# Kernel optimization log

Hardware: AMD Instinct MI355X
Metric: run time of the kernel (lower is better)

## Reference

```python
import jax, jax.numpy as jnp
import numpy as np

B, N, C_IN = 2048, 62, 512
NUM_LAYERS, H, C_OUT_PER_HEAD = 3, 8, 64


def setup_inputs() -> dict:
    key = jax.random.key(0)
    k1, k2, k3, k4 = jax.random.split(key, 4)
    x = jax.random.normal(k1, (B, N, C_IN), dtype=jnp.float32)
    L = jax.random.uniform(k2, (N, N), dtype=jnp.float32)
    W_alphas = jax.random.normal(k3, (NUM_LAYERS, H, C_IN, N), dtype=jnp.float32) * 0.05
    W = jax.random.normal(k4, (NUM_LAYERS, H, C_IN, C_OUT_PER_HEAD), dtype=jnp.float32) * 0.05
    return {"x": x, "L": L, "W_alphas": W_alphas, "W": W}


def reference(x, L, W_alphas, W):
    # x: [B, N, C]; L: [N, N]; W_alphas: [Lyr, H, C, N]; W: [Lyr, H, C, Co]
    num_layers = W_alphas.shape[0]
    n = x.shape[1]
    I = jnp.eye(n, dtype=x.dtype)
    # Chebyshev-style adjacency powers: [I, L, L@L, ...]
    adjs = [I, L]
    for _ in range(2, num_layers):
        adjs.append(adjs[-1] @ L)
    adjs = adjs[:num_layers]

    result = None
    for l in range(num_layers):
        A = adjs[l]
        A_hat = A + I
        D = A.sum(axis=-1)                      # [N]
        d_neg = jnp.where(D == 0, 0.0, 1.0 / D)  # torch: D^-1 with inf -> 0
        # attention logits per head: D_neg @ (x @ W_alphas[h]) -> [H, B, N, N]
        a = jnp.einsum('bnc,hcm->hbnm', x, W_alphas[l])
        a = d_neg[:, None] * a                   # diag(D_neg) @ M == row scaling
        a = jax.nn.leaky_relu(a, 0.01)
        a = jax.nn.softmax(a, axis=-2)           # softmax over rows (dim=-2)
        ax = jnp.einsum('nm,bmc->bnc', A_hat, x)  # A_hat @ x, shared across heads
        o = jnp.einsum('hbnm,bmc->hbnc', a, ax)
        o = jnp.einsum('hbnc,hco->hbno', o, W[l])
        o = jax.nn.relu(o)
        # concat heads along feature dim (head-major order, matching torch.cat)
        o = jnp.moveaxis(o, 0, 2).reshape(o.shape[1], n, -1)  # [B, N, H*Co]
        result = o if result is None else result + o
    return jax.nn.relu(result)
```

## Files before the change

### kernel.cpp

```cpp
#include <hip/hip_runtime.h>


using f32x4 = __attribute__((ext_vector_type(4))) float;
using s16x8 = __attribute__((ext_vector_type(8))) short;

__device__ __forceinline__ unsigned short f2bf(float f){
  unsigned int u = __builtin_bit_cast(unsigned int, f);
  u += 0x7fffu + ((u >> 16) & 1u);
  return (unsigned short)(u >> 16);
}
__device__ __forceinline__ float bf2f(unsigned short h){
  unsigned int u = ((unsigned int)h) << 16;
  return __builtin_bit_cast(float, u);
}
__device__ __forceinline__ f32x4 zf4(){ f32x4 v; v[0]=0.f; v[1]=0.f; v[2]=0.f; v[3]=0.f; return v; }

__device__ __forceinline__ void async16(const void* g, void* l){
  __builtin_amdgcn_global_load_lds((const __attribute__((address_space(1))) unsigned int*)g,
                                   (__attribute__((address_space(3))) unsigned int*)l,
                                   16, 0, 0);
}

__global__ void k_prep_adj(const float* __restrict__ L,
                           unsigned short* __restrict__ ahat,
                           float* __restrict__ dneg)
{
  __shared__ float Ls[62*62];
  __shared__ float A2s[62*62];
  const int tid = threadIdx.x;
  for (int i = tid; i < 62*62; i += 256) Ls[i] = L[i];
  __syncthreads();
  for (int i = tid; i < 62*62; i += 256){
    const int n = i / 62, m = i % 62;
    float s = 0.f;
    for (int k = 0; k < 62; ++k) s += Ls[n*62 + k] * Ls[k*62 + m];
    A2s[i] = s;
  }
  __syncthreads();
  for (int i = tid; i < 3*64*64; i += 256){
    const int l = i >> 12, r = i & 4095, n = r >> 6, m = r & 63;
    float v = 0.f;
    if (n < 62 && m < 62){
      float base = 0.f;
      if (l == 0) base = (n == m) ? 1.f : 0.f;
      else if (l == 1) base = Ls[n*62 + m];
      else base = A2s[n*62 + m];
      v = base + ((n == m) ? 1.f : 0.f);
    }
    ahat[i] = f2bf(v);
  }
  for (int i = tid; i < 3*64; i += 256){
    const int l = i >> 6, n = i & 63;
    float D = 0.f;
    if (n < 62){
      if (l == 0) D = 1.f;
      else {
        const float* src = (l == 1) ? Ls : A2s;
        for (int m = 0; m < 62; ++m) D += src[n*62 + m];
      }
    }
    dneg[i] = (D == 0.f) ? 0.f : 1.f / D;
  }
}

__global__ void k_prep_w(const float* __restrict__ Wa, const float* __restrict__ W,
                         unsigned short* __restrict__ WaT, unsigned short* __restrict__ WT)
{
  const int idx = blockIdx.x * 256 + threadIdx.x;
  if (idx < 786432){
    const int c = idx & 511, m = (idx >> 9) & 63, lh = idx >> 15;
    const float v = (m < 62) ? Wa[((size_t)lh*512 + c)*62 + m] : 0.f;
    WaT[idx] = f2bf(v);
  } else if (idx < 1572864){
    const int j = idx - 786432;
    const int c = j & 511, o = (j >> 9) & 63, lh = j >> 15;
    WT[j] = f2bf(W[((size_t)lh*512 + c)*64 + o]);
  }
}

#define LP 72

__global__ __launch_bounds__(256, 2)
void k_main(const float* __restrict__ x,
            const unsigned short* __restrict__ WaT,
            const unsigned short* __restrict__ WT,
            const unsigned short* __restrict__ ahat,
            const float* __restrict__ dneg,
            float* __restrict__ out)
{
  __shared__ __align__(16) unsigned short s_u[16384];
  __shared__ __align__(16) float s_dneg[192];
  __shared__ __align__(16) float s_red[256];
  __shared__ __align__(16) float s_red2[256];

  unsigned short* const s_chunk0 = s_u;
  unsigned short* const s_chunk1 = s_u + 8192;
  unsigned short* const s_a      = s_u;
  unsigned short* const s_xwT    = s_u + 4608;
  unsigned short* const s_axwT   = s_u + 9216;

  const int tid  = threadIdx.x;
  const int wv   = tid >> 6;
  const int lane = tid & 63;
  const int q    = lane >> 4;
  const int m15  = lane & 15;
  const int b    = blockIdx.x;
  const int r0   = 16*wv + 4*q;

  if (tid < 192) s_dneg[tid] = dneg[tid];

  s16x8 afr[16];
  {
    const int row = 16*wv + m15;
    if (row < 62){
      const float* xp = x + ((size_t)b*62 + row)*512 + q*8;
      #pragma unroll
      for (int kk = 0; kk < 16; ++kk){
        const f32x4 f0 = *(const f32x4*)(xp + kk*32);
        const f32x4 f1 = *(const f32x4*)(xp + kk*32 + 4);
        s16x8 t;
        t[0]=(short)f2bf(f0[0]); t[1]=(short)f2bf(f0[1]); t[2]=(short)f2bf(f0[2]); t[3]=(short)f2bf(f0[3]);
        t[4]=(short)f2bf(f1[0]); t[5]=(short)f2bf(f1[1]); t[6]=(short)f2bf(f1[2]); t[7]=(short)f2bf(f1[3]);
        afr[kk] = t;
      }
    } else {
      #pragma unroll
      for (int kk = 0; kk < 16; ++kk){
        s16x8 t; t[0]=0;t[1]=0;t[2]=0;t[3]=0;t[4]=0;t[5]=0;t[6]=0;t[7]=0; afr[kk] = t;
      }
    }
  }

  #pragma unroll 1
  for (int h = 0; h < 8; ++h){
    f32x4 out_acc[4];
    #pragma unroll
    for (int ct = 0; ct < 4; ++ct) out_acc[ct] = zf4();

    #pragma unroll 1
    for (int l = 0; l < 3; ++l){
      const int lh = l*8 + h;
      const unsigned short* wa_base = WaT + (size_t)lh*32768;
      const unsigned short* wt_base = WT  + (size_t)lh*32768;

      f32x4 accL[4], accX[4];
      #pragma unroll
      for (int ct = 0; ct < 4; ++ct){ accL[ct] = zf4(); accX[ct] = zf4(); }

      #pragma unroll
      for (int kc = 0; kc < 4; ++kc){
        __syncthreads();
        #pragma unroll
        for (int tt = 0; tt < 4; ++tt){
          const int n  = 16*tt + 4*wv + q;
          const int jl = m15 ^ (n & 15);
          const size_t goff = (size_t)n*512 + (size_t)kc*128 + (size_t)jl*8;
          const int    loff = tt*2048 + wv*512 + lane*8;
          async16(wa_base + goff, s_chunk0 + loff);
          async16(wt_base + goff, s_chunk1 + loff);
        }
        __syncthreads();
        #pragma unroll
        for (int ks = 0; ks < 4; ++ks){
          const s16x8 a = afr[kc*4 + ks];
          #pragma unroll
          for (int ct = 0; ct < 4; ++ct){
            const int off = (16*ct + m15)*128 + (((4*ks + q) ^ m15) * 8);
            const s16x8 bL = *(const s16x8*)(s_chunk0 + off);
            const s16x8 bX = *(const s16x8*)(s_chunk1 + off);
            accL[ct] = __builtin_amdgcn_mfma_f32_16x16x32_bf16(a, bL, accL[ct], 0, 0, 0);
            accX[ct] = __builtin_amdgcn_mfma_f32_16x16x32_bf16(a, bX, accX[ct], 0, 0, 0);
          }
        }
      }
      __syncthreads();

      {
        const f32x4 dn = *(const f32x4*)(&s_dneg[l*64 + r0]);
        #pragma unroll
        for (int ct = 0; ct < 4; ++ct){
          const int col = 16*ct + m15;
          #pragma unroll
          for (int r = 0; r < 4; ++r){
            const int n = r0 + r;
            float v = accL[ct][r] * dn[r];
            v = (v > 0.f) ? v : 0.01f*v;
            if (n >= 62) v = -1e30f;
            s_a[n*LP + col]   = f2bf(v);
            s_xwT[col*LP + n] = f2bf(accX[ct][r]);
          }
        }
      }
      __syncthreads();

      f32x4 accA[4];
      #pragma unroll
      for (int ct = 0; ct < 4; ++ct) accA[ct] = zf4();
      #pragma unroll
      for (int ks = 0; ks < 2; ++ks){
        const s16x8 aA = *(const s16x8*)(ahat + (size_t)(l*64 + 16*wv + m15)*64 + ks*32 + q*8);
        #pragma unroll
        for (int ct = 0; ct < 4; ++ct){
          const s16x8 bA = *(const s16x8*)(&s_xwT[(16*ct + m15)*LP + ks*32 + q*8]);
          accA[ct] = __builtin_amdgcn_mfma_f32_16x16x32_bf16(aA, bA, accA[ct], 0, 0, 0);
        }
      }
      #pragma unroll
      for (int ct = 0; ct < 4; ++ct){
        #pragma unroll
        for (int r = 0; r < 4; ++r)
          s_axwT[(16*ct + m15)*LP + (r0 + r)] = f2bf(accA[ct][r]);
      }

      float vsm[16];
      float mp = -3.0e38f;
      #pragma unroll
      for (int i = 0; i < 16; ++i){
        vsm[i] = bf2f(s_a[(16*wv + i)*LP + lane]);
        mp = fmaxf(mp, vsm[i]);
      }
      s_red[wv*64 + lane] = mp;
      __syncthreads();
      const float mc = fmaxf(fmaxf(s_red[lane], s_red[64 + lane]),
                             fmaxf(s_red[128 + lane], s_red[192 + lane]));
      float ev[16]; float sp = 0.f;
      #pragma unroll
      for (int i = 0; i < 16; ++i){ ev[i] = __expf(vsm[i] - mc); sp += ev[i]; }
      s_red2[wv*64 + lane] = sp;
      __syncthreads();
      const float sc = s_red2[lane] + s_red2[64 + lane] + s_red2[128 + lane] + s_red2[192 + lane];
      const float inv = 1.0f / sc;
      #pragma unroll
      for (int i = 0; i < 16; ++i)
        s_a[(16*wv + i)*LP + lane] = f2bf(ev[i] * inv);
      __syncthreads();

      f32x4 accO[4];
      #pragma unroll
      for (int ct = 0; ct < 4; ++ct) accO[ct] = zf4();
      #pragma unroll
      for (int ks = 0; ks < 2; ++ks){
        const s16x8 aO = *(const s16x8*)(&s_a[(16*wv + m15)*LP + ks*32 + q*8]);
        #pragma unroll
        for (int ct = 0; ct < 4; ++ct){
          const s16x8 bO = *(const s16x8*)(&s_axwT[(16*ct + m15)*LP + ks*32 + q*8]);
          accO[ct] = __builtin_amdgcn_mfma_f32_16x16x32_bf16(aO, bO, accO[ct], 0, 0, 0);
        }
      }
      #pragma unroll
      for (int ct = 0; ct < 4; ++ct){
        #pragma unroll
        for (int r = 0; r < 4; ++r)
          out_acc[ct][r] += fmaxf(accO[ct][r], 0.f);
      }
    }

    #pragma unroll
    for (int ct = 0; ct < 4; ++ct){
      const int col = h*64 + 16*ct + m15;
      #pragma unroll
      for (int r = 0; r < 4; ++r){
        const int n = r0 + r;
        if (n < 62)
          out[((size_t)b*62 + n)*512 + col] = fmaxf(out_acc[ct][r], 0.f);
      }
    }
  }
}

extern "C" void kernel_launch(void* const* d_in, const int* in_sizes, int n_in,
                              void* d_out, int out_size, void* d_ws, size_t ws_size,
                              hipStream_t stream)
{
  const float* x  = (const float*)d_in[0];
  const float* L  = (const float*)d_in[1];
  const float* Wa = (const float*)d_in[2];
  const float* W  = (const float*)d_in[3];
  float* out = (float*)d_out;

  char* ws = (char*)d_ws;
  unsigned short* ws_ahat = (unsigned short*)(ws);
  float*          ws_dneg = (float*)(ws + 24576);
  unsigned short* ws_WaT  = (unsigned short*)(ws + 25600);
  unsigned short* ws_WT   = (unsigned short*)(ws + 25600 + 1572864);

  k_prep_adj<<<1, 256, 0, stream>>>(L, ws_ahat, ws_dneg);
  k_prep_w<<<6144, 256, 0, stream>>>(Wa, W, ws_WaT, ws_WT);
  k_main<<<2048, 256, 0, stream>>>(x, ws_WaT, ws_WT, ws_ahat, ws_dneg, out);
}
```

Measured before the change: 1.070 ms.

## Process two batch elements per block sharing staged weight chunks

Each block now runs 512 threads as two 4-wave groups, each handling a different batch element. The groups cooperatively stage the shared Wa and W chunks into LDS, one group loading each, so every weight chunk fetched from global memory serves two batch elements and the per-block load work halves. Per-group scratch regions for the attention, xW and A·xW tiles are placed in separate LDS slices, and the softmax reductions are indexed per group. In exchange the block is larger, LDS use rises, and block-wide barriers now couple both groups, which may lower occupancy.

```diff
diff --git a/kernel.cpp b/kernel.cpp
--- a/kernel.cpp
+++ b/kernel.cpp
@@ -80,7 +80,7 @@
 
 #define LP 72
 
-__global__ __launch_bounds__(256, 2)
+__global__ __launch_bounds__(512, 2)
 void k_main(const float* __restrict__ x,
             const unsigned short* __restrict__ WaT,
             const unsigned short* __restrict__ WT,
@@ -88,30 +88,33 @@
             const float* __restrict__ dneg,
             float* __restrict__ out)
 {
-  __shared__ __align__(16) unsigned short s_u[16384];
+  __shared__ __align__(16) unsigned short s_u[27648];
   __shared__ __align__(16) float s_dneg[192];
-  __shared__ __align__(16) float s_red[256];
-  __shared__ __align__(16) float s_red2[256];
+  __shared__ __align__(16) float s_red[512];
+  __shared__ __align__(16) float s_red2[512];
 
   unsigned short* const s_chunk0 = s_u;
   unsigned short* const s_chunk1 = s_u + 8192;
-  unsigned short* const s_a      = s_u;
-  unsigned short* const s_xwT    = s_u + 4608;
-  unsigned short* const s_axwT   = s_u + 9216;
 
   const int tid  = threadIdx.x;
-  const int wv   = tid >> 6;
+  const int wv8  = tid >> 6;
+  const int grp  = wv8 >> 2;
+  const int wvg  = wv8 & 3;
   const int lane = tid & 63;
   const int q    = lane >> 4;
   const int m15  = lane & 15;
-  const int b    = blockIdx.x;
-  const int r0   = 16*wv + 4*q;
+  const int b    = 2*blockIdx.x + grp;
+  const int r0   = 16*wvg + 4*q;
+
+  unsigned short* const s_a    = s_u + grp*13824;
+  unsigned short* const s_xwT  = s_u + grp*13824 + 4608;
+  unsigned short* const s_axwT = s_u + grp*13824 + 9216;
 
   if (tid < 192) s_dneg[tid] = dneg[tid];
 
   s16x8 afr[16];
   {
-    const int row = 16*wv + m15;
+    const int row = 16*wvg + m15;
     if (row < 62){
       const float* xp = x + ((size_t)b*62 + row)*512 + q*8;
       #pragma unroll
@@ -140,8 +143,8 @@
     #pragma unroll 1
     for (int l = 0; l < 3; ++l){
       const int lh = l*8 + h;
-      const unsigned short* wa_base = WaT + (size_t)lh*32768;
-      const unsigned short* wt_base = WT  + (size_t)lh*32768;
+      const unsigned short* g_base = (grp ? WT : WaT) + (size_t)lh*32768;
+      unsigned short* const  l_base = grp ? s_chunk1 : s_chunk0;
 
       f32x4 accL[4], accX[4];
       #pragma unroll
@@ -152,12 +155,11 @@
         __syncthreads();
         #pragma unroll
         for (int tt = 0; tt < 4; ++tt){
-          const int n  = 16*tt + 4*wv + q;
+          const int n  = 16*tt + 4*wvg + q;
           const int jl = m15 ^ (n & 15);
           const size_t goff = (size_t)n*512 + (size_t)kc*128 + (size_t)jl*8;
-          const int    loff = tt*2048 + wv*512 + lane*8;
-          async16(wa_base + goff, s_chunk0 + loff);
-          async16(wt_base + goff, s_chunk1 + loff);
+          const int    loff = tt*2048 + wvg*512 + lane*8;
+          async16(g_base + goff, l_base + loff);
         }
         __syncthreads();
         #pragma unroll
@@ -198,7 +200,7 @@
       for (int ct = 0; ct < 4; ++ct) accA[ct] = zf4();
       #pragma unroll
       for (int ks = 0; ks < 2; ++ks){
-        const s16x8 aA = *(const s16x8*)(ahat + (size_t)(l*64 + 16*wv + m15)*64 + ks*32 + q*8);
+        const s16x8 aA = *(const s16x8*)(ahat + (size_t)(l*64 + 16*wvg + m15)*64 + ks*32 + q*8);
         #pragma unroll
         for (int ct = 0; ct < 4; ++ct){
           const s16x8 bA = *(const s16x8*)(&s_xwT[(16*ct + m15)*LP + ks*32 + q*8]);
@@ -216,23 +218,24 @@
       float mp = -3.0e38f;
       #pragma unroll
       for (int i = 0; i < 16; ++i){
-        vsm[i] = bf2f(s_a[(16*wv + i)*LP + lane]);
+        vsm[i] = bf2f(s_a[(16*wvg + i)*LP + lane]);
         mp = fmaxf(mp, vsm[i]);
       }
-      s_red[wv*64 + lane] = mp;
-      __syncthreads();
-      const float mc = fmaxf(fmaxf(s_red[lane], s_red[64 + lane]),
-                             fmaxf(s_red[128 + lane], s_red[192 + lane]));
+      s_red[wv8*64 + lane] = mp;
+      __syncthreads();
+      const int rb = grp*256 + lane;
+      const float mc = fmaxf(fmaxf(s_red[rb], s_red[64 + rb]),
+                             fmaxf(s_red[128 + rb], s_red[192 + rb]));
       float ev[16]; float sp = 0.f;
       #pragma unroll
       for (int i = 0; i < 16; ++i){ ev[i] = __expf(vsm[i] - mc); sp += ev[i]; }
-      s_red2[wv*64 + lane] = sp;
-      __syncthreads();
-      const float sc = s_red2[lane] + s_red2[64 + lane] + s_red2[128 + lane] + s_red2[192 + lane];
+      s_red2[wv8*64 + lane] = sp;
+      __syncthreads();
+      const float sc = s_red2[rb] + s_red2[64 + rb] + s_red2[128 + rb] + s_red2[192 + rb];
       const float inv = 1.0f / sc;
       #pragma unroll
       for (int i = 0; i < 16; ++i)
-        s_a[(16*wv + i)*LP + lane] = f2bf(ev[i] * inv);
+        s_a[(16*wvg + i)*LP + lane] = f2bf(ev[i] * inv);
       __syncthreads();
 
       f32x4 accO[4];
@@ -240,7 +243,7 @@
       for (int ct = 0; ct < 4; ++ct) accO[ct] = zf4();
       #pragma unroll
       for (int ks = 0; ks < 2; ++ks){
-        const s16x8 aO = *(const s16x8*)(&s_a[(16*wv + m15)*LP + ks*32 + q*8]);
+        const s16x8 aO = *(const s16x8*)(&s_a[(16*wvg + m15)*LP + ks*32 + q*8]);
         #pragma unroll
         for (int ct = 0; ct < 4; ++ct){
           const s16x8 bO = *(const s16x8*)(&s_axwT[(16*ct + m15)*LP + ks*32 + q*8]);
@@ -286,5 +289,5 @@
 
   k_prep_adj<<<1, 256, 0, stream>>>(L, ws_ahat, ws_dneg);
   k_prep_w<<<6144, 256, 0, stream>>>(Wa, W, ws_WaT, ws_WT);
-  k_main<<<2048, 256, 0, stream>>>(x, ws_WaT, ws_WT, ws_ahat, ws_dneg, out);
-}
+  k_main<<<1024, 512, 0, stream>>>(x, ws_WaT, ws_WT, ws_ahat, ws_dneg, out);
+}
```

Result: slower. 1.138 ms (+6.3%).

## Fold softmax normalization into A_hat·XW output and drop max subtraction

Applied to the files above, without the earlier changes.

Computes exp of the leaky-relu logits directly without subtracting the column max, and instead of normalizing the attention matrix, it scales the A_hat·(xW) rows by the reciprocal column sums before the final MFMA. This removes one reduction pass, one barrier and a rewrite of the attention tile, and packs four bf16 values per 64-bit shared-memory store. It also launches the adjacency prep kernel with 1024 threads. Skipping the max subtraction risks overflow if logits grow large.

```diff
diff --git a/kernel.cpp b/kernel.cpp
--- a/kernel.cpp
+++ b/kernel.cpp
@@ -15,6 +15,13 @@
 }
 __device__ __forceinline__ f32x4 zf4(){ f32x4 v; v[0]=0.f; v[1]=0.f; v[2]=0.f; v[3]=0.f; return v; }
 
+__device__ __forceinline__ unsigned long long pack4bf(float a, float b, float c, float d){
+  return (unsigned long long)f2bf(a)
+       | ((unsigned long long)f2bf(b) << 16)
+       | ((unsigned long long)f2bf(c) << 32)
+       | ((unsigned long long)f2bf(d) << 48);
+}
+
 __device__ __forceinline__ void async16(const void* g, void* l){
   __builtin_amdgcn_global_load_lds((const __attribute__((address_space(1))) unsigned int*)g,
                                    (__attribute__((address_space(3))) unsigned int*)l,
@@ -28,16 +35,17 @@
   __shared__ float Ls[62*62];
   __shared__ float A2s[62*62];
   const int tid = threadIdx.x;
-  for (int i = tid; i < 62*62; i += 256) Ls[i] = L[i];
+  const int NT  = blockDim.x;
+  for (int i = tid; i < 62*62; i += NT) Ls[i] = L[i];
   __syncthreads();
-  for (int i = tid; i < 62*62; i += 256){
+  for (int i = tid; i < 62*62; i += NT){
     const int n = i / 62, m = i % 62;
     float s = 0.f;
     for (int k = 0; k < 62; ++k) s += Ls[n*62 + k] * Ls[k*62 + m];
     A2s[i] = s;
   }
   __syncthreads();
-  for (int i = tid; i < 3*64*64; i += 256){
+  for (int i = tid; i < 3*64*64; i += NT){
     const int l = i >> 12, r = i & 4095, n = r >> 6, m = r & 63;
     float v = 0.f;
     if (n < 62 && m < 62){
@@ -49,7 +57,7 @@
     }
     ahat[i] = f2bf(v);
   }
-  for (int i = tid; i < 3*64; i += 256){
+  for (int i = tid; i < 3*64; i += NT){
     const int l = i >> 6, n = i & 63;
     float D = 0.f;
     if (n < 62){
@@ -91,7 +99,6 @@
   __shared__ __align__(16) unsigned short s_u[16384];
   __shared__ __align__(16) float s_dneg[192];
   __shared__ __align__(16) float s_red[256];
-  __shared__ __align__(16) float s_red2[256];
 
   unsigned short* const s_chunk0 = s_u;
   unsigned short* const s_chunk1 = s_u + 8192;
@@ -180,18 +187,27 @@
         #pragma unroll
         for (int ct = 0; ct < 4; ++ct){
           const int col = 16*ct + m15;
+          *(unsigned long long*)(&s_xwT[col*LP + r0]) =
+              pack4bf(accX[ct][0], accX[ct][1], accX[ct][2], accX[ct][3]);
           #pragma unroll
           for (int r = 0; r < 4; ++r){
             const int n = r0 + r;
             float v = accL[ct][r] * dn[r];
             v = (v > 0.f) ? v : 0.01f*v;
-            if (n >= 62) v = -1e30f;
-            s_a[n*LP + col]   = f2bf(v);
-            s_xwT[col*LP + n] = f2bf(accX[ct][r]);
+            const float e = (n < 62) ? __expf(v) : 0.f;
+            s_a[n*LP + col] = f2bf(e);
           }
         }
       }
       __syncthreads();
+
+      {
+        float sp = 0.f;
+        #pragma unroll
+        for (int i = 0; i < 16; ++i)
+          sp += bf2f(s_a[(16*wv + i)*LP + lane]);
+        s_red[wv*64 + lane] = sp;
+      }
 
       f32x4 accA[4];
       #pragma unroll
@@ -205,34 +221,23 @@
           accA[ct] = __builtin_amdgcn_mfma_f32_16x16x32_bf16(aA, bA, accA[ct], 0, 0, 0);
         }
       }
-      #pragma unroll
-      for (int ct = 0; ct < 4; ++ct){
-        #pragma unroll
-        for (int r = 0; r < 4; ++r)
-          s_axwT[(16*ct + m15)*LP + (r0 + r)] = f2bf(accA[ct][r]);
-      }
-
-      float vsm[16];
-      float mp = -3.0e38f;
-      #pragma unroll
-      for (int i = 0; i < 16; ++i){
-        vsm[i] = bf2f(s_a[(16*wv + i)*LP + lane]);
-        mp = fmaxf(mp, vsm[i]);
-      }
-      s_red[wv*64 + lane] = mp;
-      __syncthreads();
-      const float mc = fmaxf(fmaxf(s_red[lane], s_red[64 + lane]),
-                             fmaxf(s_red[128 + lane], s_red[192 + lane]));
-      float ev[16]; float sp = 0.f;
-      #pragma unroll
-      for (int i = 0; i < 16; ++i){ ev[i] = __expf(vsm[i] - mc); sp += ev[i]; }
-      s_red2[wv*64 + lane] = sp;
-      __syncthreads();
-      const float sc = s_red2[lane] + s_red2[64 + lane] + s_red2[128 + lane] + s_red2[192 + lane];
-      const float inv = 1.0f / sc;
-      #pragma unroll
-      for (int i = 0; i < 16; ++i)
-        s_a[(16*wv + i)*LP + lane] = f2bf(ev[i] * inv);
+      __syncthreads();
+
+      {
+        f32x4 inv4;
+        #pragma unroll
+        for (int r = 0; r < 4; ++r){
+          const int m = r0 + r;
+          const float S = s_red[m] + s_red[64 + m] + s_red[128 + m] + s_red[192 + m];
+          inv4[r] = 1.0f / S;
+        }
+        #pragma unroll
+        for (int ct = 0; ct < 4; ++ct){
+          *(unsigned long long*)(&s_axwT[(16*ct + m15)*LP + r0]) =
+              pack4bf(accA[ct][0]*inv4[0], accA[ct][1]*inv4[1],
+                      accA[ct][2]*inv4[2], accA[ct][3]*inv4[3]);
+        }
+      }
       __syncthreads();
 
       f32x4 accO[4];
@@ -284,7 +289,7 @@
   unsigned short* ws_WaT  = (unsigned short*)(ws + 25600);
   unsigned short* ws_WT   = (unsigned short*)(ws + 25600 + 1572864);
 
-  k_prep_adj<<<1, 256, 0, stream>>>(L, ws_ahat, ws_dneg);
+  k_prep_adj<<<1, 1024, 0, stream>>>(L, ws_ahat, ws_dneg);
   k_prep_w<<<6144, 256, 0, stream>>>(Wa, W, ws_WaT, ws_WT);
   k_main<<<2048, 256, 0, stream>>>(x, ws_WaT, ws_WT, ws_ahat, ws_dneg, out);
 }
```

Result: faster. 1.007 ms (-5.9%).
